# Kernel optimization log

Measured on AMD Instinct MI355X. Metric: run time of the kernel, lower is better.

Reference implementation:

```python
import jax, jax.numpy as jnp
import numpy as np

# irreps: 256x0e + 128x1o + 64x2e  -> feature dim 256 + 384 + 320 = 960
M0, M1, M2 = 256, 128, 64
LOG2 = float(np.log(2.0))

# e3nn normalize2mom constant for shifted-softplus: 1/sqrt(E_{z~N(0,1)}[ssp(z)^2])
_z = np.linspace(-10.0, 10.0, 200001)
_phi = np.exp(-0.5 * _z ** 2) / np.sqrt(2.0 * np.pi)
_f = np.logaddexp(0.0, _z) - LOG2
C_SSP = float(1.0 / np.sqrt(np.trapz(_f ** 2 * _phi, _z)))


def _ssp(x):
    # shifted softplus, normalized to unit second moment as in e3nn Activation
    return C_SSP * (jax.nn.softplus(x) - LOG2)


def setup_inputs() -> dict:
    key = jax.random.key(0)
    ks = jax.random.split(key, 7)
    n = 65536
    return {
        "x": jax.random.normal(ks[0], (n, M0 + 3 * M1 + 5 * M2), dtype=jnp.float32),
        # linear1: l=0 block maps 256x0e -> (256 scalars + 192 gates)x0e
        "w1_s": jax.random.normal(ks[1], (M0, M0 + M1 + M2), dtype=jnp.float32),
        "w1_v1": jax.random.normal(ks[2], (M1, M1), dtype=jnp.float32),
        "w1_v2": jax.random.normal(ks[3], (M2, M2), dtype=jnp.float32),
        # linear2: gate.irreps_out -> irreps_in
        "w2_s": jax.random.normal(ks[4], (M0, M0), dtype=jnp.float32),
        "w2_v1": jax.random.normal(ks[5], (M1, M1), dtype=jnp.float32),
        "w2_v2": jax.random.normal(ks[6], (M2, M2), dtype=jnp.float32),
    }


def reference(x, w1_s, w1_v1, w1_v2, w2_s, w2_v1, w2_v2):
    n = x.shape[0]
    # split input into irrep segments
    x0 = x[:, :M0]                                  # [n, 256] scalars (0e)
    x1 = x[:, M0:M0 + 3 * M1].reshape(n, M1, 3)     # [n, 128, 3] (1o)
    x2 = x[:, M0 + 3 * M1:].reshape(n, M2, 5)       # [n, 64, 5]  (2e)

    # linear1 (per-l block matmuls, e3nn 1/sqrt(fan_in) normalization, no bias)
    s = (x0 @ w1_s) * (1.0 / np.sqrt(M0))                   # [n, 448]
    v1 = jnp.einsum('nic,io->noc', x1, w1_v1) * (1.0 / np.sqrt(M1))
    v2 = jnp.einsum('nic,io->noc', x2, w1_v2) * (1.0 / np.sqrt(M2))

    # Gate: activate scalars, activate gates, multiply gated irreps by gates
    scalars = _ssp(s[:, :M0])          # [n, 256]
    gates = _ssp(s[:, M0:])            # [n, 192] = 128 (for 1o) + 64 (for 2e)
    v1 = v1 * gates[:, :M1, None]
    v2 = v2 * gates[:, M1:, None]

    # linear2
    y0 = (scalars @ w2_s) * (1.0 / np.sqrt(M0))
    y1 = jnp.einsum('nic,io->noc', v1, w2_v1) * (1.0 / np.sqrt(M1))
    y2 = jnp.einsum('nic,io->noc', v2, w2_v2) * (1.0 / np.sqrt(M2))

    y = jnp.concatenate([y0, y1.reshape(n, -1), y2.reshape(n, -1)], axis=1)
    return x + y  # resnet
```

## Files before the change

### kernel.cpp

```cpp
#include <hip/hip_runtime.h>
#include <math.h>

#define XP 960
typedef __attribute__((ext_vector_type(8))) short short8;
typedef __attribute__((ext_vector_type(4))) float f32x4;
typedef __attribute__((ext_vector_type(4))) float float4v;

__device__ short g_pack[221184];

__device__ __forceinline__ short f2bf(float f) {
    union { float f; unsigned u; } v; v.f = f;
    unsigned r = (v.u + 0x7fffu + ((v.u >> 16) & 1u)) >> 16;
    return (short)r;
}
__device__ __forceinline__ float bf2f(short s) {
    union { float f; unsigned u; } v;
    v.u = ((unsigned)(unsigned short)s) << 16;
    return v.f;
}
__device__ __forceinline__ float ssp(float v, float c) {
    float sp = fmaxf(v, 0.f) + log1pf(expf(-fabsf(v)));
    return c * (sp - 0.69314718055994531f);
}

__global__ void pack_weights(const float* __restrict__ w1s, const float* __restrict__ w1v1,
                             const float* __restrict__ w1v2, const float* __restrict__ w2s,
                             const float* __restrict__ w2v1, const float* __restrict__ w2v2) {
    int g = blockIdx.x * blockDim.x + threadIdx.x;
    const float* src; int NT, N, dstoff, lg;
    if      (g < 14336) { src = w1s;  NT = 28; N = 448; dstoff = 0;      lg = g; }
    else if (g < 16384) { src = w1v1; NT = 8;  N = 128; dstoff = 114688; lg = g - 14336; }
    else if (g < 16896) { src = w1v2; NT = 4;  N = 64;  dstoff = 131072; lg = g - 16384; }
    else if (g < 25088) { src = w2s;  NT = 16; N = 256; dstoff = 135168; lg = g - 16896; }
    else if (g < 27136) { src = w2v1; NT = 8;  N = 128; dstoff = 200704; lg = g - 25088; }
    else if (g < 27648) { src = w2v2; NT = 4;  N = 64;  dstoff = 217088; lg = g - 27136; }
    else return;
    int lane = lg & 63;
    int t = lg >> 6;
    int nt = t % NT;
    int kt = t / NT;
    int k0 = kt * 32 + (lane >> 4) * 8;
    int n  = nt * 16 + (lane & 15);
    short* dst = g_pack + dstoff + (size_t)lg * 8;
#pragma unroll
    for (int j = 0; j < 8; j++) dst[j] = f2bf(src[(size_t)(k0 + j) * N + n]);
}

#define MFMA(a, b, c) __builtin_amdgcn_mfma_f32_16x16x32_bf16((a), (b), (c), 0, 0, 0)

__global__ __launch_bounds__(256, 4) void fused_kernel(const float* __restrict__ x,
                                                       float* __restrict__ out,
                                                       float c_ssp) {
    __shared__ __align__(16) short sstage[4][16 * 264];
    __shared__ __align__(16) short gstage[4][16 * 200];

    const int lane = threadIdx.x & 63;
    const int wave = threadIdx.x >> 6;
    const int q = lane >> 4, l15 = lane & 15;
    const int row0 = blockIdx.x * 64 + wave * 16;

    short* ss = sstage[wave];
    short* gs = gstage[wave];

    const short8* pw1s  = (const short8*)(g_pack + 0);
    const short8* pw1v1 = (const short8*)(g_pack + 114688);
    const short8* pw1v2 = (const short8*)(g_pack + 131072);
    const short8* pw2s  = (const short8*)(g_pack + 135168);
    const short8* pw2v1 = (const short8*)(g_pack + 200704);
    const short8* pw2v2 = (const short8*)(g_pack + 217088);

    const float* xa = x + (size_t)(row0 + l15) * XP;
    const float* xr = x + (size_t)row0 * XP;
    float* yr = out + (size_t)row0 * XP;

    const float s1  = 0.0625f;
    const float sv1 = 0.08838834764831845f;
    const float sv2 = 0.125f;

    short8 a0[8];
#pragma unroll
    for (int kt = 0; kt < 8; kt++) {
        const float* p = xa + kt * 32 + q * 8;
        float4v u0 = *(const float4v*)p;
        float4v u1 = *(const float4v*)(p + 4);
        short8 f;
        f[0] = f2bf(u0[0]); f[1] = f2bf(u0[1]); f[2] = f2bf(u0[2]); f[3] = f2bf(u0[3]);
        f[4] = f2bf(u1[0]); f[5] = f2bf(u1[1]); f[6] = f2bf(u1[2]); f[7] = f2bf(u1[3]);
        a0[kt] = f;
    }

#pragma unroll 1
    for (int np = 0; np < 14; np++) {
        f32x4 acc0 = {0.f, 0.f, 0.f, 0.f}, acc1 = {0.f, 0.f, 0.f, 0.f};
#pragma unroll
        for (int kt = 0; kt < 8; kt++) {
            short8 b0 = pw1s[(kt * 28 + 2 * np + 0) * 64 + lane];
            short8 b1 = pw1s[(kt * 28 + 2 * np + 1) * 64 + lane];
            acc0 = MFMA(a0[kt], b0, acc0);
            acc1 = MFMA(a0[kt], b1, acc1);
        }
#pragma unroll
        for (int half = 0; half < 2; half++) {
            f32x4 a = half ? acc1 : acc0;
            int col = (2 * np + half) * 16 + l15;
#pragma unroll
            for (int r = 0; r < 4; r++) {
                short bv = f2bf(ssp(a[r] * s1, c_ssp));
                if (col < 256) ss[(q * 4 + r) * 264 + col] = bv;
                else           gs[(q * 4 + r) * 200 + (col - 256)] = bv;
            }
        }
    }
    __syncthreads();

    {
        short8 as[8];
#pragma unroll
        for (int kt = 0; kt < 8; kt++)
            as[kt] = *(const short8*)&ss[l15 * 264 + kt * 32 + q * 8];
#pragma unroll 1
        for (int np = 0; np < 8; np++) {
            f32x4 acc0 = {0.f, 0.f, 0.f, 0.f}, acc1 = {0.f, 0.f, 0.f, 0.f};
#pragma unroll
            for (int kt = 0; kt < 8; kt++) {
                short8 b0 = pw2s[(kt * 16 + 2 * np + 0) * 64 + lane];
                short8 b1 = pw2s[(kt * 16 + 2 * np + 1) * 64 + lane];
                acc0 = MFMA(as[kt], b0, acc0);
                acc1 = MFMA(as[kt], b1, acc1);
            }
#pragma unroll
            for (int half = 0; half < 2; half++) {
                f32x4 a = half ? acc1 : acc0;
                int col = (2 * np + half) * 16 + l15;
#pragma unroll
                for (int r = 0; r < 4; r++) {
                    size_t off = (size_t)(q * 4 + r) * XP + col;
                    yr[off] = xr[off] + a[r] * s1;
                }
            }
        }
    }

#pragma unroll 1
    for (int c = 0; c < 3; c++) {
        short8 a1[4];
#pragma unroll
        for (int kt = 0; kt < 4; kt++) {
            short8 f;
#pragma unroll
            for (int j = 0; j < 8; j++) {
                int i = kt * 32 + q * 8 + j;
                f[j] = f2bf(xa[256 + i * 3 + c]);
            }
            a1[kt] = f;
        }
        __syncthreads();
#pragma unroll 1
        for (int np = 0; np < 4; np++) {
            f32x4 acc0 = {0.f, 0.f, 0.f, 0.f}, acc1 = {0.f, 0.f, 0.f, 0.f};
#pragma unroll
            for (int kt = 0; kt < 4; kt++) {
                short8 b0 = pw1v1[(kt * 8 + 2 * np + 0) * 64 + lane];
                short8 b1 = pw1v1[(kt * 8 + 2 * np + 1) * 64 + lane];
                acc0 = MFMA(a1[kt], b0, acc0);
                acc1 = MFMA(a1[kt], b1, acc1);
            }
#pragma unroll
            for (int half = 0; half < 2; half++) {
                f32x4 a = half ? acc1 : acc0;
                int o = (2 * np + half) * 16 + l15;
#pragma unroll
                for (int r = 0; r < 4; r++) {
                    float g = bf2f(gs[(q * 4 + r) * 200 + o]);
                    ss[(q * 4 + r) * 136 + o] = f2bf(a[r] * sv1 * g);
                }
            }
        }
        __syncthreads();
        short8 av[4];
#pragma unroll
        for (int kt = 0; kt < 4; kt++)
            av[kt] = *(const short8*)&ss[l15 * 136 + kt * 32 + q * 8];
#pragma unroll 1
        for (int np = 0; np < 4; np++) {
            f32x4 acc0 = {0.f, 0.f, 0.f, 0.f}, acc1 = {0.f, 0.f, 0.f, 0.f};
#pragma unroll
            for (int kt = 0; kt < 4; kt++) {
                short8 b0 = pw2v1[(kt * 8 + 2 * np + 0) * 64 + lane];
                short8 b1 = pw2v1[(kt * 8 + 2 * np + 1) * 64 + lane];
                acc0 = MFMA(av[kt], b0, acc0);
                acc1 = MFMA(av[kt], b1, acc1);
            }
#pragma unroll
            for (int half = 0; half < 2; half++) {
                f32x4 a = half ? acc1 : acc0;
                int o = (2 * np + half) * 16 + l15;
#pragma unroll
                for (int r = 0; r < 4; r++) {
                    size_t off = (size_t)(q * 4 + r) * XP + 256 + o * 3 + c;
                    yr[off] = xr[off] + a[r] * sv1;
                }
            }
        }
    }

#pragma unroll 1
    for (int c = 0; c < 5; c++) {
        short8 a2[2];
#pragma unroll
        for (int kt = 0; kt < 2; kt++) {
            short8 f;
#pragma unroll
            for (int j = 0; j < 8; j++) {
                int i = kt * 32 + q * 8 + j;
                f[j] = f2bf(xa[640 + i * 5 + c]);
            }
            a2[kt] = f;
        }
        __syncthreads();
#pragma unroll 1
        for (int np = 0; np < 2; np++) {
            f32x4 acc0 = {0.f, 0.f, 0.f, 0.f}, acc1 = {0.f, 0.f, 0.f, 0.f};
#pragma unroll
            for (int kt = 0; kt < 2; kt++) {
                short8 b0 = pw1v2[(kt * 4 + 2 * np + 0) * 64 + lane];
                short8 b1 = pw1v2[(kt * 4 + 2 * np + 1) * 64 + lane];
                acc0 = MFMA(a2[kt], b0, acc0);
                acc1 = MFMA(a2[kt], b1, acc1);
            }
#pragma unroll
            for (int half = 0; half < 2; half++) {
                f32x4 a = half ? acc1 : acc0;
                int o = (2 * np + half) * 16 + l15;
#pragma unroll
                for (int r = 0; r < 4; r++) {
                    float g = bf2f(gs[(q * 4 + r) * 200 + 128 + o]);
                    ss[(q * 4 + r) * 72 + o] = f2bf(a[r] * sv2 * g);
                }
            }
        }
        __syncthreads();
        short8 av[2];
#pragma unroll
        for (int kt = 0; kt < 2; kt++)
            av[kt] = *(const short8*)&ss[l15 * 72 + kt * 32 + q * 8];
#pragma unroll 1
        for (int np = 0; np < 2; np++) {
            f32x4 acc0 = {0.f, 0.f, 0.f, 0.f}, acc1 = {0.f, 0.f, 0.f, 0.f};
#pragma unroll
            for (int kt = 0; kt < 2; kt++) {
                short8 b0 = pw2v2[(kt * 4 + 2 * np + 0) * 64 + lane];
                short8 b1 = pw2v2[(kt * 4 + 2 * np + 1) * 64 + lane];
                acc0 = MFMA(av[kt], b0, acc0);
                acc1 = MFMA(av[kt], b1, acc1);
            }
#pragma unroll
            for (int half = 0; half < 2; half++) {
                f32x4 a = half ? acc1 : acc0;
                int o = (2 * np + half) * 16 + l15;
#pragma unroll
                for (int r = 0; r < 4; r++) {
                    size_t off = (size_t)(q * 4 + r) * XP + 640 + o * 5 + c;
                    yr[off] = xr[off] + a[r] * sv2;
                }
            }
        }
    }
}

static float compute_cssp() {
    const int N = 200001;
    const double dz = 20.0 / 200000.0;
    double sum = 0.0;
    for (int i = 0; i < N; i++) {
        double z = -10.0 + dz * i;
        double f = (z > 0 ? z : 0.0) + log1p(exp(-fabs(z))) - 0.69314718055994530942;
        double phi = exp(-0.5 * z * z) * 0.39894228040143267794;
        double y = f * f * phi;
        sum += (i == 0 || i == N - 1) ? 0.5 * y : y;
    }
    return (float)(1.0 / sqrt(sum * dz));
}

extern "C" void kernel_launch(void* const* d_in, const int* in_sizes, int n_in,
                              void* d_out, int out_size, void* d_ws, size_t ws_size,
                              hipStream_t stream) {
    const float* x    = (const float*)d_in[0];
    const float* w1s  = (const float*)d_in[1];
    const float* w1v1 = (const float*)d_in[2];
    const float* w1v2 = (const float*)d_in[3];
    const float* w2s  = (const float*)d_in[4];
    const float* w2v1 = (const float*)d_in[5];
    const float* w2v2 = (const float*)d_in[6];
    float* out = (float*)d_out;

    static const float c_ssp = compute_cssp();

    int rows = in_sizes[0] / XP;
    int blocks = rows / 64;

    pack_weights<<<108, 256, 0, stream>>>(w1s, w1v1, w1v2, w2s, w2v1, w2v2);
    fused_kernel<<<blocks, 256, 0, stream>>>(x, out, c_ssp);
}
```

Measured before the change: 768.1 us.

## Rewrite fused gate kernel with transposed MFMA, register gates, vectorized IO

Swaps the MFMA operand order so each lane owns a whole output row. This lets the residual add and output writes use contiguous float4 nontemporal loads and stores in place of strided scalar accesses. Gate activations stay in registers instead of LDS, and the 1o/2e inputs are loaded once with vector loads and deinterleaved per component. Block-wide __syncthreads are replaced by per-wave lgkmcnt waits, softplus uses exp2/log2 intrinsics, bf16 packing is simplified to round-half-up, and launch bounds drop to 3 blocks per CU. Higher register pressure and slightly less accurate activation and rounding are the trade-offs.

```diff
diff --git a/kernel.cpp b/kernel.cpp
--- a/kernel.cpp
+++ b/kernel.cpp
@@ -4,7 +4,8 @@
 #define XP 960
 typedef __attribute__((ext_vector_type(8))) short short8;
 typedef __attribute__((ext_vector_type(4))) float f32x4;
-typedef __attribute__((ext_vector_type(4))) float float4v;
+typedef __attribute__((ext_vector_type(4))) float fv4;
+typedef __attribute__((ext_vector_type(4))) unsigned uint4v;
 
 __device__ short g_pack[221184];
 
@@ -13,15 +14,25 @@
     unsigned r = (v.u + 0x7fffu + ((v.u >> 16) & 1u)) >> 16;
     return (short)r;
 }
-__device__ __forceinline__ float bf2f(short s) {
-    union { float f; unsigned u; } v;
-    v.u = ((unsigned)(unsigned short)s) << 16;
-    return v.f;
+__device__ __forceinline__ unsigned pk2(float a, float b) {
+    union { float f; unsigned u; } x, y; x.f = a; y.f = b;
+    return ((x.u + 0x8000u) >> 16) | ((y.u + 0x8000u) & 0xffff0000u);
+}
+__device__ __forceinline__ short8 mk8(unsigned d0, unsigned d1, unsigned d2, unsigned d3) {
+    union { uint4v u; short8 s; } cv;
+    cv.u = (uint4v){d0, d1, d2, d3};
+    return cv.s;
 }
 __device__ __forceinline__ float ssp(float v, float c) {
-    float sp = fmaxf(v, 0.f) + log1pf(expf(-fabsf(v)));
-    return c * (sp - 0.69314718055994531f);
-}
+    float t = exp2f(fabsf(v) * -1.44269504088896340736f);
+    float sp = fmaxf(v, 0.f) + 0.69314718055994530942f * __log2f(1.0f + t);
+    return c * (sp - 0.69314718055994530942f);
+}
+
+#define WSYNC() asm volatile("s_waitcnt lgkmcnt(0)" ::: "memory")
+#define MFMA(a, b, c) __builtin_amdgcn_mfma_f32_16x16x32_bf16((a), (b), (c), 0, 0, 0)
+#define NTL(p) __builtin_nontemporal_load((const fv4*)(p))
+#define NTS(p, v) __builtin_nontemporal_store((v), (fv4*)(p))
 
 __global__ void pack_weights(const float* __restrict__ w1s, const float* __restrict__ w1v1,
                              const float* __restrict__ w1v2, const float* __restrict__ w2s,
@@ -46,21 +57,19 @@
     for (int j = 0; j < 8; j++) dst[j] = f2bf(src[(size_t)(k0 + j) * N + n]);
 }
 
-#define MFMA(a, b, c) __builtin_amdgcn_mfma_f32_16x16x32_bf16((a), (b), (c), 0, 0, 0)
-
-__global__ __launch_bounds__(256, 4) void fused_kernel(const float* __restrict__ x,
+__global__ __launch_bounds__(256, 3) void fused_kernel(const float* __restrict__ x,
                                                        float* __restrict__ out,
                                                        float c_ssp) {
-    __shared__ __align__(16) short sstage[4][16 * 264];
-    __shared__ __align__(16) short gstage[4][16 * 200];
+    __shared__ __align__(16) short arena[4][16 * 408];
 
     const int lane = threadIdx.x & 63;
     const int wave = threadIdx.x >> 6;
     const int q = lane >> 4, l15 = lane & 15;
     const int row0 = blockIdx.x * 64 + wave * 16;
-
-    short* ss = sstage[wave];
-    short* gs = gstage[wave];
+    short* S = arena[wave];
+    unsigned* Sd = (unsigned*)S;
+    const int dwb = l15 * 204 + q * 2;
+    const short* Sr = S + l15 * 408 + q * 8;
 
     const short8* pw1s  = (const short8*)(g_pack + 0);
     const short8* pw1v1 = (const short8*)(g_pack + 114688);
@@ -69,202 +78,192 @@
     const short8* pw2v1 = (const short8*)(g_pack + 200704);
     const short8* pw2v2 = (const short8*)(g_pack + 217088);
 
-    const float* xa = x + (size_t)(row0 + l15) * XP;
-    const float* xr = x + (size_t)row0 * XP;
-    float* yr = out + (size_t)row0 * XP;
-
-    const float s1  = 0.0625f;
-    const float sv1 = 0.08838834764831845f;
-    const float sv2 = 0.125f;
-
-    short8 a0[8];
+    const float* xrow = x + (size_t)(row0 + l15) * XP;
+    float* yrow = out + (size_t)(row0 + l15) * XP;
+
+    const float S1  = 0.0625f;
+    const float SV1 = 0.08838834764831845f;
+    const float SV2 = 0.125f;
+
+    short8 xf0[8];
 #pragma unroll
     for (int kt = 0; kt < 8; kt++) {
-        const float* p = xa + kt * 32 + q * 8;
-        float4v u0 = *(const float4v*)p;
-        float4v u1 = *(const float4v*)(p + 4);
-        short8 f;
-        f[0] = f2bf(u0[0]); f[1] = f2bf(u0[1]); f[2] = f2bf(u0[2]); f[3] = f2bf(u0[3]);
-        f[4] = f2bf(u1[0]); f[5] = f2bf(u1[1]); f[6] = f2bf(u1[2]); f[7] = f2bf(u1[3]);
-        a0[kt] = f;
+        fv4 u0 = *(const fv4*)(xrow + kt * 32 + q * 8);
+        fv4 u1 = *(const fv4*)(xrow + kt * 32 + q * 8 + 4);
+        xf0[kt] = mk8(pk2(u0[0], u0[1]), pk2(u0[2], u0[3]), pk2(u1[0], u1[1]), pk2(u1[2], u1[3]));
     }
 
 #pragma unroll 1
-    for (int np = 0; np < 14; np++) {
-        f32x4 acc0 = {0.f, 0.f, 0.f, 0.f}, acc1 = {0.f, 0.f, 0.f, 0.f};
+    for (int tp = 0; tp < 8; tp++) {
+        f32x4 a0 = {0.f,0.f,0.f,0.f}, a1 = {0.f,0.f,0.f,0.f};
 #pragma unroll
         for (int kt = 0; kt < 8; kt++) {
-            short8 b0 = pw1s[(kt * 28 + 2 * np + 0) * 64 + lane];
-            short8 b1 = pw1s[(kt * 28 + 2 * np + 1) * 64 + lane];
-            acc0 = MFMA(a0[kt], b0, acc0);
-            acc1 = MFMA(a0[kt], b1, acc1);
-        }
-#pragma unroll
-        for (int half = 0; half < 2; half++) {
-            f32x4 a = half ? acc1 : acc0;
-            int col = (2 * np + half) * 16 + l15;
-#pragma unroll
-            for (int r = 0; r < 4; r++) {
-                short bv = f2bf(ssp(a[r] * s1, c_ssp));
-                if (col < 256) ss[(q * 4 + r) * 264 + col] = bv;
-                else           gs[(q * 4 + r) * 200 + (col - 256)] = bv;
+            a0 = MFMA(pw1s[(kt * 28 + 2 * tp + 0) * 64 + lane], xf0[kt], a0);
+            a1 = MFMA(pw1s[(kt * 28 + 2 * tp + 1) * 64 + lane], xf0[kt], a1);
+        }
+#pragma unroll
+        for (int h = 0; h < 2; h++) {
+            f32x4 a = h ? a1 : a0;
+            int t = 2 * tp + h;
+            Sd[dwb + t * 8]     = pk2(ssp(a[0] * S1, c_ssp), ssp(a[1] * S1, c_ssp));
+            Sd[dwb + t * 8 + 1] = pk2(ssp(a[2] * S1, c_ssp), ssp(a[3] * S1, c_ssp));
+        }
+    }
+    f32x4 gacc[12];
+#pragma unroll
+    for (int tp = 0; tp < 6; tp++) {
+        f32x4 a0 = {0.f,0.f,0.f,0.f}, a1 = {0.f,0.f,0.f,0.f};
+#pragma unroll
+        for (int kt = 0; kt < 8; kt++) {
+            a0 = MFMA(pw1s[(kt * 28 + 16 + 2 * tp + 0) * 64 + lane], xf0[kt], a0);
+            a1 = MFMA(pw1s[(kt * 28 + 16 + 2 * tp + 1) * 64 + lane], xf0[kt], a1);
+        }
+        gacc[2 * tp]     = (f32x4){ssp(a0[0]*S1,c_ssp), ssp(a0[1]*S1,c_ssp), ssp(a0[2]*S1,c_ssp), ssp(a0[3]*S1,c_ssp)};
+        gacc[2 * tp + 1] = (f32x4){ssp(a1[0]*S1,c_ssp), ssp(a1[1]*S1,c_ssp), ssp(a1[2]*S1,c_ssp), ssp(a1[3]*S1,c_ssp)};
+    }
+    WSYNC();
+
+    short8 sf[8];
+#pragma unroll
+    for (int kt = 0; kt < 8; kt++) sf[kt] = *(const short8*)(Sr + kt * 32);
+#pragma unroll 1
+    for (int tp = 0; tp < 8; tp++) {
+        f32x4 a0 = {0.f,0.f,0.f,0.f}, a1 = {0.f,0.f,0.f,0.f};
+#pragma unroll
+        for (int kt = 0; kt < 8; kt++) {
+            a0 = MFMA(pw2s[(kt * 16 + 2 * tp + 0) * 64 + lane], sf[kt], a0);
+            a1 = MFMA(pw2s[(kt * 16 + 2 * tp + 1) * 64 + lane], sf[kt], a1);
+        }
+#pragma unroll
+        for (int h = 0; h < 2; h++) {
+            f32x4 a = h ? a1 : a0;
+            int col = (2 * tp + h) * 16 + q * 4;
+            fv4 r = NTL(xrow + col);
+            fv4 o = {r[0] + a[0] * S1, r[1] + a[1] * S1, r[2] + a[2] * S1, r[3] + a[3] * S1};
+            NTS(yrow + col, o);
+        }
+    }
+
+    short8 xf1[3][4];
+#pragma unroll
+    for (int kt = 0; kt < 4; kt++) {
+        float b[24];
+        const float* p = xrow + 256 + 3 * (kt * 32 + q * 8);
+#pragma unroll
+        for (int i = 0; i < 6; i++) *(fv4*)(b + 4 * i) = *(const fv4*)(p + 4 * i);
+#pragma unroll
+        for (int c = 0; c < 3; c++)
+            xf1[c][kt] = mk8(pk2(b[c], b[c+3]), pk2(b[c+6], b[c+9]),
+                             pk2(b[c+12], b[c+15]), pk2(b[c+18], b[c+21]));
+    }
+#pragma unroll
+    for (int c = 0; c < 3; c++) {
+#pragma unroll
+        for (int tp = 0; tp < 4; tp++) {
+            f32x4 a0 = {0.f,0.f,0.f,0.f}, a1 = {0.f,0.f,0.f,0.f};
+#pragma unroll
+            for (int kt = 0; kt < 4; kt++) {
+                a0 = MFMA(pw1v1[(kt * 8 + 2 * tp + 0) * 64 + lane], xf1[c][kt], a0);
+                a1 = MFMA(pw1v1[(kt * 8 + 2 * tp + 1) * 64 + lane], xf1[c][kt], a1);
             }
-        }
-    }
-    __syncthreads();
-
-    {
-        short8 as[8];
-#pragma unroll
-        for (int kt = 0; kt < 8; kt++)
-            as[kt] = *(const short8*)&ss[l15 * 264 + kt * 32 + q * 8];
+#pragma unroll
+            for (int h = 0; h < 2; h++) {
+                f32x4 a = h ? a1 : a0;
+                int t = 2 * tp + h;
+                f32x4 g = gacc[t];
+                Sd[dwb + c * 68 + t * 8]     = pk2(a[0]*SV1*g[0], a[1]*SV1*g[1]);
+                Sd[dwb + c * 68 + t * 8 + 1] = pk2(a[2]*SV1*g[2], a[3]*SV1*g[3]);
+            }
+        }
+    }
+    WSYNC();
+    short8 vf[3][4];
+#pragma unroll
+    for (int c = 0; c < 3; c++)
+#pragma unroll
+        for (int kt = 0; kt < 4; kt++)
+            vf[c][kt] = *(const short8*)(Sr + c * 136 + kt * 32);
 #pragma unroll 1
-        for (int np = 0; np < 8; np++) {
-            f32x4 acc0 = {0.f, 0.f, 0.f, 0.f}, acc1 = {0.f, 0.f, 0.f, 0.f};
-#pragma unroll
-            for (int kt = 0; kt < 8; kt++) {
-                short8 b0 = pw2s[(kt * 16 + 2 * np + 0) * 64 + lane];
-                short8 b1 = pw2s[(kt * 16 + 2 * np + 1) * 64 + lane];
-                acc0 = MFMA(as[kt], b0, acc0);
-                acc1 = MFMA(as[kt], b1, acc1);
+    for (int t = 0; t < 8; t++) {
+        f32x4 ac0 = {0.f,0.f,0.f,0.f}, ac1 = {0.f,0.f,0.f,0.f}, ac2 = {0.f,0.f,0.f,0.f};
+#pragma unroll
+        for (int kt = 0; kt < 4; kt++) {
+            short8 w = pw2v1[(kt * 8 + t) * 64 + lane];
+            ac0 = MFMA(w, vf[0][kt], ac0);
+            ac1 = MFMA(w, vf[1][kt], ac1);
+            ac2 = MFMA(w, vf[2][kt], ac2);
+        }
+        int base = 256 + 3 * (t * 16 + q * 4);
+        fv4 r0 = NTL(xrow + base), r1 = NTL(xrow + base + 4), r2 = NTL(xrow + base + 8);
+        fv4 o0 = {r0[0]+ac0[0]*SV1, r0[1]+ac1[0]*SV1, r0[2]+ac2[0]*SV1, r0[3]+ac0[1]*SV1};
+        fv4 o1 = {r1[0]+ac1[1]*SV1, r1[1]+ac2[1]*SV1, r1[2]+ac0[2]*SV1, r1[3]+ac1[2]*SV1};
+        fv4 o2 = {r2[0]+ac2[2]*SV1, r2[1]+ac0[3]*SV1, r2[2]+ac1[3]*SV1, r2[3]+ac2[3]*SV1};
+        NTS(yrow + base, o0); NTS(yrow + base + 4, o1); NTS(yrow + base + 8, o2);
+    }
+
+    short8 xf2[5][2];
+#pragma unroll
+    for (int kt = 0; kt < 2; kt++) {
+        float b[40];
+        const float* p = xrow + 640 + 5 * (kt * 32 + q * 8);
+#pragma unroll
+        for (int i = 0; i < 10; i++) *(fv4*)(b + 4 * i) = *(const fv4*)(p + 4 * i);
+#pragma unroll
+        for (int c = 0; c < 5; c++)
+            xf2[c][kt] = mk8(pk2(b[c], b[c+5]), pk2(b[c+10], b[c+15]),
+                             pk2(b[c+20], b[c+25]), pk2(b[c+30], b[c+35]));
+    }
+#pragma unroll
+    for (int c = 0; c < 5; c++) {
+#pragma unroll
+        for (int tp = 0; tp < 2; tp++) {
+            f32x4 a0 = {0.f,0.f,0.f,0.f}, a1 = {0.f,0.f,0.f,0.f};
+#pragma unroll
+            for (int kt = 0; kt < 2; kt++) {
+                a0 = MFMA(pw1v2[(kt * 4 + 2 * tp + 0) * 64 + lane], xf2[c][kt], a0);
+                a1 = MFMA(pw1v2[(kt * 4 + 2 * tp + 1) * 64 + lane], xf2[c][kt], a1);
             }
 #pragma unroll
-            for (int half = 0; half < 2; half++) {
-                f32x4 a = half ? acc1 : acc0;
-                int col = (2 * np + half) * 16 + l15;
-#pragma unroll
-                for (int r = 0; r < 4; r++) {
-                    size_t off = (size_t)(q * 4 + r) * XP + col;
-                    yr[off] = xr[off] + a[r] * s1;
-                }
+            for (int h = 0; h < 2; h++) {
+                f32x4 a = h ? a1 : a0;
+                int t = 2 * tp + h;
+                f32x4 g = gacc[8 + t];
+                Sd[dwb + c * 36 + t * 8]     = pk2(a[0]*SV2*g[0], a[1]*SV2*g[1]);
+                Sd[dwb + c * 36 + t * 8 + 1] = pk2(a[2]*SV2*g[2], a[3]*SV2*g[3]);
             }
         }
     }
-
+    WSYNC();
+    short8 vf2[5][2];
+#pragma unroll
+    for (int c = 0; c < 5; c++)
+#pragma unroll
+        for (int kt = 0; kt < 2; kt++)
+            vf2[c][kt] = *(const short8*)(Sr + c * 72 + kt * 32);
 #pragma unroll 1
-    for (int c = 0; c < 3; c++) {
-        short8 a1[4];
-#pragma unroll
-        for (int kt = 0; kt < 4; kt++) {
-            short8 f;
-#pragma unroll
-            for (int j = 0; j < 8; j++) {
-                int i = kt * 32 + q * 8 + j;
-                f[j] = f2bf(xa[256 + i * 3 + c]);
-            }
-            a1[kt] = f;
-        }
-        __syncthreads();
-#pragma unroll 1
-        for (int np = 0; np < 4; np++) {
-            f32x4 acc0 = {0.f, 0.f, 0.f, 0.f}, acc1 = {0.f, 0.f, 0.f, 0.f};
-#pragma unroll
-            for (int kt = 0; kt < 4; kt++) {
-                short8 b0 = pw1v1[(kt * 8 + 2 * np + 0) * 64 + lane];
-                short8 b1 = pw1v1[(kt * 8 + 2 * np + 1) * 64 + lane];
-                acc0 = MFMA(a1[kt], b0, acc0);
-                acc1 = MFMA(a1[kt], b1, acc1);
-            }
-#pragma unroll
-            for (int half = 0; half < 2; half++) {
-                f32x4 a = half ? acc1 : acc0;
-                int o = (2 * np + half) * 16 + l15;
-#pragma unroll
-                for (int r = 0; r < 4; r++) {
-                    float g = bf2f(gs[(q * 4 + r) * 200 + o]);
-                    ss[(q * 4 + r) * 136 + o] = f2bf(a[r] * sv1 * g);
-                }
-            }
-        }
-        __syncthreads();
-        short8 av[4];
-#pragma unroll
-        for (int kt = 0; kt < 4; kt++)
-            av[kt] = *(const short8*)&ss[l15 * 136 + kt * 32 + q * 8];
-#pragma unroll 1
-        for (int np = 0; np < 4; np++) {
-            f32x4 acc0 = {0.f, 0.f, 0.f, 0.f}, acc1 = {0.f, 0.f, 0.f, 0.f};
-#pragma unroll
-            for (int kt = 0; kt < 4; kt++) {
-                short8 b0 = pw2v1[(kt * 8 + 2 * np + 0) * 64 + lane];
-                short8 b1 = pw2v1[(kt * 8 + 2 * np + 1) * 64 + lane];
-                acc0 = MFMA(av[kt], b0, acc0);
-                acc1 = MFMA(av[kt], b1, acc1);
-            }
-#pragma unroll
-            for (int half = 0; half < 2; half++) {
-                f32x4 a = half ? acc1 : acc0;
-                int o = (2 * np + half) * 16 + l15;
-#pragma unroll
-                for (int r = 0; r < 4; r++) {
-                    size_t off = (size_t)(q * 4 + r) * XP + 256 + o * 3 + c;
-                    yr[off] = xr[off] + a[r] * sv1;
-                }
-            }
-        }
-    }
-
-#pragma unroll 1
-    for (int c = 0; c < 5; c++) {
-        short8 a2[2];
+    for (int t = 0; t < 4; t++) {
+        f32x4 b0 = {0.f,0.f,0.f,0.f}, b1 = {0.f,0.f,0.f,0.f}, b2 = {0.f,0.f,0.f,0.f},
+              b3 = {0.f,0.f,0.f,0.f}, b4 = {0.f,0.f,0.f,0.f};
 #pragma unroll
         for (int kt = 0; kt < 2; kt++) {
-            short8 f;
-#pragma unroll
-            for (int j = 0; j < 8; j++) {
-                int i = kt * 32 + q * 8 + j;
-                f[j] = f2bf(xa[640 + i * 5 + c]);
-            }
-            a2[kt] = f;
-        }
-        __syncthreads();
-#pragma unroll 1
-        for (int np = 0; np < 2; np++) {
-            f32x4 acc0 = {0.f, 0.f, 0.f, 0.f}, acc1 = {0.f, 0.f, 0.f, 0.f};
-#pragma unroll
-            for (int kt = 0; kt < 2; kt++) {
-                short8 b0 = pw1v2[(kt * 4 + 2 * np + 0) * 64 + lane];
-                short8 b1 = pw1v2[(kt * 4 + 2 * np + 1) * 64 + lane];
-                acc0 = MFMA(a2[kt], b0, acc0);
-                acc1 = MFMA(a2[kt], b1, acc1);
-            }
-#pragma unroll
-            for (int half = 0; half < 2; half++) {
-                f32x4 a = half ? acc1 : acc0;
-                int o = (2 * np + half) * 16 + l15;
-#pragma unroll
-                for (int r = 0; r < 4; r++) {
-                    float g = bf2f(gs[(q * 4 + r) * 200 + 128 + o]);
-                    ss[(q * 4 + r) * 72 + o] = f2bf(a[r] * sv2 * g);
-                }
-            }
-        }
-        __syncthreads();
-        short8 av[2];
-#pragma unroll
-        for (int kt = 0; kt < 2; kt++)
-            av[kt] = *(const short8*)&ss[l15 * 72 + kt * 32 + q * 8];
-#pragma unroll 1
-        for (int np = 0; np < 2; np++) {
-            f32x4 acc0 = {0.f, 0.f, 0.f, 0.f}, acc1 = {0.f, 0.f, 0.f, 0.f};
-#pragma unroll
-            for (int kt = 0; kt < 2; kt++) {
-                short8 b0 = pw2v2[(kt * 4 + 2 * np + 0) * 64 + lane];
-                short8 b1 = pw2v2[(kt * 4 + 2 * np + 1) * 64 + lane];
-                acc0 = MFMA(av[kt], b0, acc0);
-                acc1 = MFMA(av[kt], b1, acc1);
-            }
-#pragma unroll
-            for (int half = 0; half < 2; half++) {
-                f32x4 a = half ? acc1 : acc0;
-                int o = (2 * np + half) * 16 + l15;
-#pragma unroll
-                for (int r = 0; r < 4; r++) {
-                    size_t off = (size_t)(q * 4 + r) * XP + 640 + o * 5 + c;
-                    yr[off] = xr[off] + a[r] * sv2;
-                }
-            }
-        }
+            short8 w = pw2v2[(kt * 4 + t) * 64 + lane];
+            b0 = MFMA(w, vf2[0][kt], b0);
+            b1 = MFMA(w, vf2[1][kt], b1);
+            b2 = MFMA(w, vf2[2][kt], b2);
+            b3 = MFMA(w, vf2[3][kt], b3);
+            b4 = MFMA(w, vf2[4][kt], b4);
+        }
+        int base = 640 + 5 * (t * 16 + q * 4);
+        fv4 r0 = NTL(xrow + base),      r1 = NTL(xrow + base + 4),
+            r2 = NTL(xrow + base + 8),  r3 = NTL(xrow + base + 12),
+            r4 = NTL(xrow + base + 16);
+        fv4 o0 = {r0[0]+b0[0]*SV2, r0[1]+b1[0]*SV2, r0[2]+b2[0]*SV2, r0[3]+b3[0]*SV2};
+        fv4 o1 = {r1[0]+b4[0]*SV2, r1[1]+b0[1]*SV2, r1[2]+b1[1]*SV2, r1[3]+b2[1]*SV2};
+        fv4 o2 = {r2[0]+b3[1]*SV2, r2[1]+b4[1]*SV2, r2[2]+b0[2]*SV2, r2[3]+b1[2]*SV2};
+        fv4 o3 = {r3[0]+b2[2]*SV2, r3[1]+b3[2]*SV2, r3[2]+b4[2]*SV2, r3[3]+b0[3]*SV2};
+        fv4 o4 = {r4[0]+b1[3]*SV2, r4[1]+b2[3]*SV2, r4[2]+b3[3]*SV2, r4[3]+b4[3]*SV2};
+        NTS(yrow + base, o0); NTS(yrow + base + 4, o1); NTS(yrow + base + 8, o2);
+        NTS(yrow + base + 12, o3); NTS(yrow + base + 16, o4);
     }
 }
 
```

Measured after the change: 625.8 us. -18.5%, faster.
